# Kernel tuning notes

Hardware: AMD Instinct MI355X
Metric: run time of the kernel (lower is better)

## Reference

```python
import jax, jax.numpy as jnp
import numpy as np

B, D_INNER, D_STATE, DT_RANK = 1024, 2560, 16, 160


def setup_inputs() -> dict:
    key = jax.random.key(0)
    ks = jax.random.split(key, 9)
    s = lambda n: 1.0 / np.sqrt(n)
    return {
        "x": jax.random.normal(ks[0], (B, D_INNER), jnp.float32),
        "h": jax.random.normal(ks[1], (B, D_INNER, D_STATE), jnp.float32),
        "W_dt_low": jax.random.normal(ks[2], (DT_RANK, D_INNER), jnp.float32) * s(D_INNER),
        "W_dt": jax.random.normal(ks[3], (D_INNER, DT_RANK), jnp.float32) * s(DT_RANK),
        "b_dt": jax.random.normal(ks[4], (D_INNER,), jnp.float32),
        "W_B": jax.random.normal(ks[5], (D_STATE, D_INNER), jnp.float32) * s(D_INNER),
        "W_C": jax.random.normal(ks[6], (D_STATE, D_INNER), jnp.float32) * s(D_INNER),
        "A_log": jax.random.uniform(ks[7], (D_INNER, D_STATE), jnp.float32, 0.0, 1.0),
        "D": jax.random.normal(ks[8], (D_INNER,), jnp.float32),
    }


def reference(x, h, W_dt_low, W_dt, b_dt, W_B, W_C, A_log, D):
    # Single-token Mamba selective-scan step (decode).
    # dt projections: d_inner -> dt_rank -> d_inner, then softplus
    dt = jax.nn.softplus(jnp.einsum('bd,rd->br', x, W_dt_low) @ W_dt.T + b_dt)  # [B, D_INNER]
    Bt = jnp.einsum('bd,nd->bn', x, W_B)  # [B, D_STATE]
    Ct = jnp.einsum('bd,nd->bn', x, W_C)  # [B, D_STATE]
    A = -jnp.exp(A_log)                   # [D_INNER, D_STATE]
    delta_A = jnp.exp(dt[:, :, None] * A[None])                 # [B, D_INNER, D_STATE]
    delta_B_x = dt[:, :, None] * Bt[:, None, :] * x[:, :, None] # [B, D_INNER, D_STATE]
    h_new = delta_A * h + delta_B_x
    y = jnp.einsum('bdn,bn->bd', h_new, Ct) + D * x             # [B, D_INNER]
    return y
```

## Files before the change

kernel.cpp:

```cpp
#include <hip/hip_runtime.h>
#include <hip/hip_bf16.h>
#include <math.h>

#define B_SZ    1024
#define DI      2560
#define DS      16
#define DR      160
#define NPROJ   192

typedef __bf16 bf16x8 __attribute__((ext_vector_type(8)));
typedef __bf16 bf16x4 __attribute__((ext_vector_type(4)));
typedef float  f32x4  __attribute__((ext_vector_type(4)));

__device__ __forceinline__ void cvt4(const float* __restrict__ s,
                                     __bf16* __restrict__ d, int i) {
  float4 v = *(const float4*)(s + i);
  bf16x4 o = { (__bf16)v.x, (__bf16)v.y, (__bf16)v.z, (__bf16)v.w };
  *(bf16x4*)(d + i) = o;
}

__global__ void __launch_bounds__(256) convert_kernel(
    const float* __restrict__ x, const float* __restrict__ Wdl,
    const float* __restrict__ WB, const float* __restrict__ WC,
    const float* __restrict__ Wdt, const float* __restrict__ A_log,
    __bf16* __restrict__ xb, __bf16* __restrict__ wcat,
    __bf16* __restrict__ wdtb, float* __restrict__ negA) {
  int i = (blockIdx.x * 256 + threadIdx.x) * 4;
  const int NX   = B_SZ * DI;
  const int NWDL = DR * DI;
  const int NWB  = DS * DI;
  const int NWDT = DI * DR;
  const int NA   = DI * DS;
  if (i < NX)   { cvt4(x, xb, i); return; }
  i -= NX;
  if (i < NWDL) { cvt4(Wdl, wcat, i); return; }
  i -= NWDL;
  if (i < NWB)  { cvt4(WB, wcat + NWDL, i); return; }
  i -= NWB;
  if (i < NWB)  { cvt4(WC, wcat + NWDL + NWB, i); return; }
  i -= NWB;
  if (i < NWDT) { cvt4(Wdt, wdtb, i); return; }
  i -= NWDT;
  if (i < NA) {
    float4 v = *(const float4*)(A_log + i);
    float4 o = { -__expf(v.x), -__expf(v.y), -__expf(v.z), -__expf(v.w) };
    *(float4*)(negA + i) = o;
  }
}

__global__ void __launch_bounds__(256) proj_kernel(
    const __bf16* __restrict__ xb, const __bf16* __restrict__ wcat,
    __bf16* __restrict__ dtlow, float* __restrict__ Bt, float* __restrict__ Ct) {
  int gw    = blockIdx.x * 4 + (threadIdx.x >> 6);
  int lane  = threadIdx.x & 63;
  int mtile = gw & 63;
  int ntile = gw >> 6;
  int b0 = mtile * 16, n0 = ntile * 16;
  int m = lane & 15, quad = lane >> 4;
  const __bf16* ap = xb   + (size_t)(b0 + m) * DI + quad * 8;
  const __bf16* bp = wcat + (size_t)(n0 + m) * DI + quad * 8;
  f32x4 acc = {0.f, 0.f, 0.f, 0.f};
  for (int k0 = 0; k0 < DI; k0 += 32) {
    bf16x8 a = *(const bf16x8*)(ap + k0);
    bf16x8 b = *(const bf16x8*)(bp + k0);
    acc = __builtin_amdgcn_mfma_f32_16x16x32_bf16(a, b, acc, 0, 0, 0);
  }
  int nn = n0 + m;
#pragma unroll
  for (int r = 0; r < 4; ++r) {
    int bb = b0 + quad * 4 + r;
    float v = acc[r];
    if (nn < DR)            dtlow[bb * DR + nn] = (__bf16)v;
    else if (nn < DR + DS)  Bt[bb * DS + (nn - DR)] = v;
    else                    Ct[bb * DS + (nn - DR - DS)] = v;
  }
}

__global__ void __launch_bounds__(256) dtssm_kernel(
    const __bf16* __restrict__ dtlow, const __bf16* __restrict__ wdtb,
    const float* __restrict__ b_dt,
    const float* __restrict__ x, const float* __restrict__ h,
    const float* __restrict__ negA, const float* __restrict__ Bt,
    const float* __restrict__ Ct, const float* __restrict__ Dp,
    float* __restrict__ y) {
  int gw    = blockIdx.x * 4 + (threadIdx.x >> 6);
  int lane  = threadIdx.x & 63;
  int mtile = gw & 63;
  int ntile = gw >> 6;
  int b0 = mtile * 16, d0 = ntile * 16;
  int m = lane & 15, quad = lane >> 4;
  const __bf16* ap = dtlow + (size_t)(b0 + m) * DR + quad * 8;
  const __bf16* bp = wdtb  + (size_t)(d0 + m) * DR + quad * 8;
  f32x4 acc = {0.f, 0.f, 0.f, 0.f};
#pragma unroll
  for (int k0 = 0; k0 < DR; k0 += 32) {
    bf16x8 a = *(const bf16x8*)(ap + k0);
    bf16x8 b = *(const bf16x8*)(bp + k0);
    acc = __builtin_amdgcn_mfma_f32_16x16x32_bf16(a, b, acc, 0, 0, 0);
  }
  int dd = d0 + m;
  float bias = b_dt[dd];
  float dval = Dp[dd];
  const float4* a4 = (const float4*)(negA + (size_t)dd * DS);
  float4 av0 = a4[0], av1 = a4[1], av2 = a4[2], av3 = a4[3];
#pragma unroll
  for (int r = 0; r < 4; ++r) {
    int bb = b0 + quad * 4 + r;
    size_t e = (size_t)bb * DI + dd;
    float z = acc[r] + bias;
    float dtv = (z > 20.f) ? z : log1pf(__expf(z));
    float xv  = x[e];
    float dtl = dtv * 1.44269504f;
    float dxv = dtv * xv;
    const float4* h4 = (const float4*)(h  + e * DS);
    const float4* b4 = (const float4*)(Bt + (size_t)bb * DS);
    const float4* c4 = (const float4*)(Ct + (size_t)bb * DS);
    float s = 0.f;
    {
      float4 hv = h4[0], bv = b4[0], cv = c4[0];
      s += (exp2f(av0.x * dtl) * hv.x + bv.x * dxv) * cv.x;
      s += (exp2f(av0.y * dtl) * hv.y + bv.y * dxv) * cv.y;
      s += (exp2f(av0.z * dtl) * hv.z + bv.z * dxv) * cv.z;
      s += (exp2f(av0.w * dtl) * hv.w + bv.w * dxv) * cv.w;
    }
    {
      float4 hv = h4[1], bv = b4[1], cv = c4[1];
      s += (exp2f(av1.x * dtl) * hv.x + bv.x * dxv) * cv.x;
      s += (exp2f(av1.y * dtl) * hv.y + bv.y * dxv) * cv.y;
      s += (exp2f(av1.z * dtl) * hv.z + bv.z * dxv) * cv.z;
      s += (exp2f(av1.w * dtl) * hv.w + bv.w * dxv) * cv.w;
    }
    {
      float4 hv = h4[2], bv = b4[2], cv = c4[2];
      s += (exp2f(av2.x * dtl) * hv.x + bv.x * dxv) * cv.x;
      s += (exp2f(av2.y * dtl) * hv.y + bv.y * dxv) * cv.y;
      s += (exp2f(av2.z * dtl) * hv.z + bv.z * dxv) * cv.z;
      s += (exp2f(av2.w * dtl) * hv.w + bv.w * dxv) * cv.w;
    }
    {
      float4 hv = h4[3], bv = b4[3], cv = c4[3];
      s += (exp2f(av3.x * dtl) * hv.x + bv.x * dxv) * cv.x;
      s += (exp2f(av3.y * dtl) * hv.y + bv.y * dxv) * cv.y;
      s += (exp2f(av3.z * dtl) * hv.z + bv.z * dxv) * cv.z;
      s += (exp2f(av3.w * dtl) * hv.w + bv.w * dxv) * cv.w;
    }
    y[e] = s + dval * xv;
  }
}

extern "C" void kernel_launch(void* const* d_in, const int* in_sizes, int n_in,
                              void* d_out, int out_size, void* d_ws, size_t ws_size,
                              hipStream_t stream) {
  const float* x     = (const float*)d_in[0];
  const float* h     = (const float*)d_in[1];
  const float* Wdl   = (const float*)d_in[2];
  const float* Wdt   = (const float*)d_in[3];
  const float* b_dt  = (const float*)d_in[4];
  const float* WB    = (const float*)d_in[5];
  const float* WC    = (const float*)d_in[6];
  const float* A_log = (const float*)d_in[7];
  const float* Dp    = (const float*)d_in[8];
  float* y = (float*)d_out;

  char* ws = (char*)d_ws;
  __bf16* xb    = (__bf16*)(ws);
  __bf16* wcat  = (__bf16*)(ws + 5242880);
  __bf16* wdtb  = (__bf16*)(ws + 6225920);
  float*  negA  = (float*) (ws + 7045120);
  __bf16* dtlow = (__bf16*)(ws + 7208960);
  float*  Bt    = (float*) (ws + 7536640);
  float*  Ct    = (float*) (ws + 7602176);
  if (ws_size < 7667712) return;

  convert_kernel<<<3480, 256, 0, stream>>>(x, Wdl, WB, WC, Wdt, A_log,
                                           xb, wcat, wdtb, negA);
  proj_kernel<<<192, 256, 0, stream>>>(xb, wcat, dtlow, Bt, Ct);
  dtssm_kernel<<<2560, 256, 0, stream>>>(dtlow, wdtb, b_dt, x, h, negA,
                                         Bt, Ct, Dp, y);
}
```

Measured before the change: 286.9 us.

## Fuse x bf16 conversion into projection GEMM and use 32x32 MFMA tiles

Removes the separate pass that converts x to bf16 in workspace. The projection kernel now reads fp32 x directly and converts it in registers before each MFMA. It also switches from 16x16x32 to 32x32x16 MFMA, with one wave per 32x32 tile, which gives more reuse per load. This saves a 10MB read and 5MB write of x, but the projection now reads fp32 x, which is twice the bytes, and runs only 192 single-wave blocks with a long K loop.

Result: slower. 340.7 us (+18.7%).

```diff
diff --git a/kernel.cpp b/kernel.cpp
--- a/kernel.cpp
+++ b/kernel.cpp
@@ -11,6 +11,7 @@
 typedef __bf16 bf16x8 __attribute__((ext_vector_type(8)));
 typedef __bf16 bf16x4 __attribute__((ext_vector_type(4)));
 typedef float  f32x4  __attribute__((ext_vector_type(4)));
+typedef float  f32x16 __attribute__((ext_vector_type(16)));
 
 __device__ __forceinline__ void cvt4(const float* __restrict__ s,
                                      __bf16* __restrict__ d, int i) {
@@ -20,19 +21,16 @@
 }
 
 __global__ void __launch_bounds__(256) convert_kernel(
-    const float* __restrict__ x, const float* __restrict__ Wdl,
-    const float* __restrict__ WB, const float* __restrict__ WC,
-    const float* __restrict__ Wdt, const float* __restrict__ A_log,
-    __bf16* __restrict__ xb, __bf16* __restrict__ wcat,
-    __bf16* __restrict__ wdtb, float* __restrict__ negA) {
+    const float* __restrict__ Wdl, const float* __restrict__ WB,
+    const float* __restrict__ WC, const float* __restrict__ Wdt,
+    const float* __restrict__ A_log,
+    __bf16* __restrict__ wcat, __bf16* __restrict__ wdtb,
+    float* __restrict__ negA) {
   int i = (blockIdx.x * 256 + threadIdx.x) * 4;
-  const int NX   = B_SZ * DI;
   const int NWDL = DR * DI;
   const int NWB  = DS * DI;
   const int NWDT = DI * DR;
   const int NA   = DI * DS;
-  if (i < NX)   { cvt4(x, xb, i); return; }
-  i -= NX;
   if (i < NWDL) { cvt4(Wdl, wcat, i); return; }
   i -= NWDL;
   if (i < NWB)  { cvt4(WB, wcat + NWDL, i); return; }
@@ -48,27 +46,30 @@
   }
 }
 
-__global__ void __launch_bounds__(256) proj_kernel(
-    const __bf16* __restrict__ xb, const __bf16* __restrict__ wcat,
+__global__ void __launch_bounds__(64) proj_kernel(
+    const float* __restrict__ x, const __bf16* __restrict__ wcat,
     __bf16* __restrict__ dtlow, float* __restrict__ Bt, float* __restrict__ Ct) {
-  int gw    = blockIdx.x * 4 + (threadIdx.x >> 6);
-  int lane  = threadIdx.x & 63;
-  int mtile = gw & 63;
-  int ntile = gw >> 6;
-  int b0 = mtile * 16, n0 = ntile * 16;
-  int m = lane & 15, quad = lane >> 4;
-  const __bf16* ap = xb   + (size_t)(b0 + m) * DI + quad * 8;
-  const __bf16* bp = wcat + (size_t)(n0 + m) * DI + quad * 8;
-  f32x4 acc = {0.f, 0.f, 0.f, 0.f};
-  for (int k0 = 0; k0 < DI; k0 += 32) {
-    bf16x8 a = *(const bf16x8*)(ap + k0);
+  int lane  = threadIdx.x;
+  int mtile = blockIdx.x & 31;
+  int ntile = blockIdx.x >> 5;
+  int b0 = mtile * 32, n0 = ntile * 32;
+  int r32 = lane & 31, hf = lane >> 5;
+  const float*  ap = x    + (size_t)(b0 + r32) * DI + hf * 8;
+  const __bf16* bp = wcat + (size_t)(n0 + r32) * DI + hf * 8;
+  f32x16 acc = {0.f,0.f,0.f,0.f,0.f,0.f,0.f,0.f,0.f,0.f,0.f,0.f,0.f,0.f,0.f,0.f};
+#pragma unroll 4
+  for (int k0 = 0; k0 < DI; k0 += 16) {
+    float4 a0 = *(const float4*)(ap + k0);
+    float4 a1 = *(const float4*)(ap + k0 + 4);
+    bf16x8 a = { (__bf16)a0.x, (__bf16)a0.y, (__bf16)a0.z, (__bf16)a0.w,
+                 (__bf16)a1.x, (__bf16)a1.y, (__bf16)a1.z, (__bf16)a1.w };
     bf16x8 b = *(const bf16x8*)(bp + k0);
-    acc = __builtin_amdgcn_mfma_f32_16x16x32_bf16(a, b, acc, 0, 0, 0);
+    acc = __builtin_amdgcn_mfma_f32_32x32x16_bf16(a, b, acc, 0, 0, 0);
   }
-  int nn = n0 + m;
+  int nn = n0 + r32;
 #pragma unroll
-  for (int r = 0; r < 4; ++r) {
-    int bb = b0 + quad * 4 + r;
+  for (int r = 0; r < 16; ++r) {
+    int bb = b0 + (r & 3) + 8 * (r >> 2) + 4 * hf;
     float v = acc[r];
     if (nn < DR)            dtlow[bb * DR + nn] = (__bf16)v;
     else if (nn < DR + DS)  Bt[bb * DS + (nn - DR)] = v;
@@ -163,18 +164,17 @@
   float* y = (float*)d_out;
 
   char* ws = (char*)d_ws;
-  __bf16* xb    = (__bf16*)(ws);
-  __bf16* wcat  = (__bf16*)(ws + 5242880);
-  __bf16* wdtb  = (__bf16*)(ws + 6225920);
-  float*  negA  = (float*) (ws + 7045120);
-  __bf16* dtlow = (__bf16*)(ws + 7208960);
-  float*  Bt    = (float*) (ws + 7536640);
-  float*  Ct    = (float*) (ws + 7602176);
-  if (ws_size < 7667712) return;
+  __bf16* wcat  = (__bf16*)(ws);
+  __bf16* wdtb  = (__bf16*)(ws + 983040);
+  float*  negA  = (float*) (ws + 1802240);
+  __bf16* dtlow = (__bf16*)(ws + 1966080);
+  float*  Bt    = (float*) (ws + 2293760);
+  float*  Ct    = (float*) (ws + 2359296);
+  if (ws_size < 2424832) return;
 
-  convert_kernel<<<3480, 256, 0, stream>>>(x, Wdl, WB, WC, Wdt, A_log,
-                                           xb, wcat, wdtb, negA);
-  proj_kernel<<<192, 256, 0, stream>>>(xb, wcat, dtlow, Bt, Ct);
+  convert_kernel<<<920, 256, 0, stream>>>(Wdl, WB, WC, Wdt, A_log,
+                                          wcat, wdtb, negA);
+  proj_kernel<<<192, 64, 0, stream>>>(x, wcat, dtlow, Bt, Ct);
   dtssm_kernel<<<2560, 256, 0, stream>>>(dtlow, wdtb, b_dt, x, h, negA,
                                          Bt, Ct, Dp, y);
 }
```
